# Kernel tuning notes

Measured on AMD Instinct MI355X. Metric: run time of the kernel, lower is better.

Reference implementation:

```python
import jax, jax.numpy as jnp
import numpy as np

D_MODEL = 256
NEG_INF = -1e9  # matches masked_fill value in the torch module


def setup_inputs() -> dict:
    key = jax.random.key(0)
    ks = jax.random.split(key, 7)
    B, S, D = 4, 4096, D_MODEL
    enc_q = jax.random.normal(ks[0], (B, S, D), dtype=jnp.float32)
    enc_k = jax.random.normal(ks[1], (B, S, D), dtype=jnp.float32)
    enc_v = jax.random.normal(ks[2], (B, S, D), dtype=jnp.float32)
    mask = jax.random.randint(ks[3], (B, S, S), 0, 2).astype(jnp.bool_)
    scale = 1.0 / np.sqrt(D)
    W_q = jax.random.normal(ks[4], (D, D), dtype=jnp.float32) * scale
    W_k = jax.random.normal(ks[5], (D, D), dtype=jnp.float32) * scale
    W_v = jax.random.normal(ks[6], (D, D), dtype=jnp.float32) * scale
    return {"encodings_q": enc_q, "encodings_k": enc_k, "encodings_v": enc_v,
            "mask": mask, "W_q": W_q, "W_k": W_k, "W_v": W_v}


def reference(encodings_q, encodings_k, encodings_v, mask, W_q, W_k, W_v):
    # nn.Linear(bias=False): y = x @ W^T
    q = jnp.einsum('bsd,ed->bse', encodings_q, W_q)
    k = jnp.einsum('bsd,ed->bse', encodings_k, W_k)
    v = jnp.einsum('bsd,ed->bse', encodings_v, W_v)
    sims = jnp.einsum('bqd,bkd->bqk', q, k) / jnp.sqrt(jnp.float32(D_MODEL))
    sims = jnp.where(mask, jnp.float32(NEG_INF), sims)
    attn = jax.nn.softmax(sims, axis=-1)
    return jnp.einsum('bqk,bkd->bqd', attn, v)
```

## Files before the change

kernel.cpp:

```cpp
#include <hip/hip_runtime.h>
#include <hip/hip_bf16.h>
#include <stdint.h>


typedef __attribute__((ext_vector_type(8))) short bf16x8;
typedef __attribute__((ext_vector_type(4))) float f32x4;

__device__ __forceinline__ short f2bf(float f) {
    union { float f; uint32_t u; } v; v.f = f;
    uint32_t r = v.u + 0x7FFFu + ((v.u >> 16) & 1u);
    return (short)(r >> 16);
}
__device__ __forceinline__ float bf2f(short s) {
    union { uint32_t u; float f; } v; v.u = ((uint32_t)(uint16_t)s) << 16;
    return v.f;
}

__global__ __launch_bounds__(512, 2)
void proj_kernel(const float* __restrict__ encq,
                 const float* __restrict__ enck,
                 const float* __restrict__ encv,
                 const float* __restrict__ Wq,
                 const float* __restrict__ Wk,
                 const float* __restrict__ Wv,
                 short* __restrict__ q_out,
                 short* __restrict__ k_out,
                 short* __restrict__ vt_out)
{
    __shared__ short As[128][72];
    __shared__ short Bs[256][72];

    const int tid = threadIdx.x;
    const int wave = tid >> 6, lane = tid & 63, lo = lane & 15, hi = lane >> 4;
    const int proj = blockIdx.y;
    const int row0 = blockIdx.x * 128;

    const float* X = (proj == 0) ? encq : (proj == 1) ? enck : encv;
    const float* W = (proj == 0) ? Wq   : (proj == 1) ? Wk   : Wv;

    f32x4 acc[16];
    #pragma unroll
    for (int n = 0; n < 16; ++n) {
        f32x4 z = {0.f, 0.f, 0.f, 0.f};
        acc[n] = z;
    }

    for (int ks = 0; ks < 4; ++ks) {
        const int k0 = ks * 64;
        __syncthreads();
        #pragma unroll
        for (int i = 0; i < 4; ++i) {
            int u = tid + i * 512;
            int r = u >> 4, c4 = u & 15;
            float4 v = *(const float4*)(X + (size_t)(row0 + r) * 256 + k0 + c4 * 4);
            short* dst = &As[r][c4 * 4];
            dst[0] = f2bf(v.x); dst[1] = f2bf(v.y); dst[2] = f2bf(v.z); dst[3] = f2bf(v.w);
        }
        #pragma unroll
        for (int i = 0; i < 8; ++i) {
            int u = tid + i * 512;
            int r = u >> 4, c4 = u & 15;
            float4 v = *(const float4*)(W + (size_t)r * 256 + k0 + c4 * 4);
            short* dst = &Bs[r][c4 * 4];
            dst[0] = f2bf(v.x); dst[1] = f2bf(v.y); dst[2] = f2bf(v.z); dst[3] = f2bf(v.w);
        }
        __syncthreads();
        #pragma unroll
        for (int kl = 0; kl < 2; ++kl) {
            bf16x8 a = *(const bf16x8*)&As[wave * 16 + lo][kl * 32 + hi * 8];
            #pragma unroll
            for (int n = 0; n < 16; ++n) {
                bf16x8 b = *(const bf16x8*)&Bs[n * 16 + lo][kl * 32 + hi * 8];
                acc[n] = __builtin_amdgcn_mfma_f32_16x16x32_bf16(a, b, acc[n], 0, 0, 0);
            }
        }
    }

    #pragma unroll
    for (int n = 0; n < 16; ++n)
        #pragma unroll
        for (int j = 0; j < 4; ++j) {
            int srow = row0 + wave * 16 + hi * 4 + j;
            int e = n * 16 + lo;
            float v = acc[n][j];
            if (proj == 0) {
                q_out[(size_t)srow * 256 + e] = f2bf(v * 0.0625f);
            } else if (proj == 1) {
                k_out[(size_t)srow * 256 + e] = f2bf(v);
            } else {
                int b = srow >> 12, s = srow & 4095;
                vt_out[((size_t)b * 256 + e) * 4096 + s] = f2bf(v);
            }
        }
}

__global__ __launch_bounds__(512, 2)
void attn_kernel(const short* __restrict__ qs,
                 const short* __restrict__ kk_,
                 const short* __restrict__ vt,
                 const int*   __restrict__ mask,
                 short* __restrict__ Opart,
                 float* __restrict__ Mpart,
                 float* __restrict__ Lpart)
{
    __shared__ short Ks[64 * 256];
    __shared__ short Vs[256 * 64];
    __shared__ short Ps[8][16][40];
    __shared__ unsigned long long Mb[128];

    const int tid = threadIdx.x;
    const int wave = tid >> 6, lane = tid & 63, lo = lane & 15, hi = lane >> 4;
    const int qt = blockIdx.x, b = blockIdx.y, split = blockIdx.z;
    const int qrow0 = qt * 128 + wave * 16;
    const size_t qg0 = (size_t)b * 4096 + qrow0;
    const int kv0 = split * 1024;

    bf16x8 qf[8];
    #pragma unroll
    for (int kk = 0; kk < 8; ++kk)
        qf[kk] = *(const bf16x8*)(qs + (qg0 + lo) * 256 + kk * 32 + hi * 8);

    f32x4 oacc[16];
    #pragma unroll
    for (int n = 0; n < 16; ++n) {
        f32x4 z = {0.f, 0.f, 0.f, 0.f};
        oacc[n] = z;
    }
    float Mst[4], Lst[4];
    #pragma unroll
    for (int j = 0; j < 4; ++j) { Mst[j] = -1e30f; Lst[j] = 0.f; }

    bf16x8 onesf;
    #pragma unroll
    for (int i = 0; i < 8; ++i) onesf[i] = (short)0x3F80;

    const short* ksrc0 = kk_ + ((size_t)b * 4096 + kv0) * 256;
    const size_t vbase = (size_t)b * 256 * 4096;
    const int mrow = tid >> 2, mpart = tid & 3;
    const int* msrc0 = mask + (size_t)b * 4096 * 4096
                     + (size_t)(qt * 128 + mrow) * 4096 + kv0 + mpart * 16;

    bf16x8 kreg[4], vreg[4];
    int4 mreg[4];
    #pragma unroll
    for (int i = 0; i < 4; ++i) {
        int u = tid + i * 512;
        kreg[i] = *(const bf16x8*)(ksrc0 + u * 8);
    }
    #pragma unroll
    for (int i = 0; i < 4; ++i) {
        int u = tid + i * 512;
        int r = u >> 3, cu = u & 7;
        vreg[i] = *(const bf16x8*)(vt + vbase + (size_t)r * 4096 + kv0 + cu * 8);
    }
    #pragma unroll
    for (int i = 0; i < 4; ++i)
        mreg[i] = *(const int4*)(msrc0 + i * 4);

    for (int t = 0; t < 16; ++t) {
        __syncthreads();
        #pragma unroll
        for (int i = 0; i < 4; ++i) {
            int u = tid + i * 512;
            int row = u >> 5, unit = u & 31;
            *(bf16x8*)&Ks[row * 256 + (unit ^ (row & 7)) * 8] = kreg[i];
        }
        #pragma unroll
        for (int i = 0; i < 4; ++i) {
            int u = tid + i * 512;
            int r = u >> 3, cu = u & 7;
            *(bf16x8*)&Vs[r * 64 + (cu ^ (r & 7)) * 8] = vreg[i];
        }
        {
            uint32_t mb = 0;
            #pragma unroll
            for (int i = 0; i < 4; ++i) {
                mb |= (uint32_t)(mreg[i].x != 0) << (i * 4);
                mb |= (uint32_t)(mreg[i].y != 0) << (i * 4 + 1);
                mb |= (uint32_t)(mreg[i].z != 0) << (i * 4 + 2);
                mb |= (uint32_t)(mreg[i].w != 0) << (i * 4 + 3);
            }
            ((unsigned short*)&Mb[mrow])[mpart] = (unsigned short)mb;
        }
        __syncthreads();

        if (t < 15) {
            const short* src = ksrc0 + (size_t)(t + 1) * 64 * 256;
            #pragma unroll
            for (int i = 0; i < 4; ++i) {
                int u = tid + i * 512;
                kreg[i] = *(const bf16x8*)(src + u * 8);
            }
            const int c0 = kv0 + (t + 1) * 64;
            #pragma unroll
            for (int i = 0; i < 4; ++i) {
                int u = tid + i * 512;
                int r = u >> 3, cu = u & 7;
                vreg[i] = *(const bf16x8*)(vt + vbase + (size_t)r * 4096 + c0 + cu * 8);
            }
            const int* ms = msrc0 + (t + 1) * 64;
            #pragma unroll
            for (int i = 0; i < 4; ++i)
                mreg[i] = *(const int4*)(ms + i * 4);
        }

        unsigned long long wls[4];
        #pragma unroll
        for (int j = 0; j < 4; ++j)
            wls[j] = Mb[wave * 16 + hi * 4 + j] >> lo;

        f32x4 sacc[4];
        #pragma unroll
        for (int n = 0; n < 4; ++n) {
            f32x4 z = {0.f, 0.f, 0.f, 0.f};
            sacc[n] = z;
        }
        #pragma unroll
        for (int kk = 0; kk < 8; ++kk) {
            #pragma unroll
            for (int n = 0; n < 4; ++n) {
                int row = n * 16 + lo;
                bf16x8 bk = *(const bf16x8*)&Ks[row * 256 + ((kk * 4 + hi) ^ (lo & 7)) * 8];
                sacc[n] = __builtin_amdgcn_mfma_f32_16x16x32_bf16(qf[kk], bk, sacc[n], 0, 0, 0);
            }
        }

        float ml[4];
        #pragma unroll
        for (int j = 0; j < 4; ++j) {
            float mx = -1e30f;
            #pragma unroll
            for (int n = 0; n < 4; ++n) {
                float s = sacc[n][j];
                if ((wls[j] >> (n * 16)) & 1ull) s = -1e30f;
                mx = fmaxf(mx, s);
            }
            #pragma unroll
            for (int d = 1; d < 16; d <<= 1)
                mx = fmaxf(mx, __shfl_xor(mx, d));
            ml[j] = mx;
        }

        bool needl = false;
        #pragma unroll
        for (int j = 0; j < 4; ++j)
            needl = needl || (ml[j] > Mst[j] + 8.0f);
        if (__any((int)needl)) {
            #pragma unroll
            for (int j = 0; j < 4; ++j) {
                float Mn = fmaxf(Mst[j], ml[j]);
                float sc = __expf(Mst[j] - Mn);
                Mst[j] = Mn;
                Lst[j] *= sc;
                #pragma unroll
                for (int n = 0; n < 16; ++n) oacc[n][j] *= sc;
            }
        }

        f32x4 lacc = {0.f, 0.f, 0.f, 0.f};
        #pragma unroll
        for (int g = 0; g < 2; ++g) {
            #pragma unroll
            for (int nn = 0; nn < 2; ++nn) {
                int n = g * 2 + nn;
                #pragma unroll
                for (int j = 0; j < 4; ++j) {
                    float p = __expf(sacc[n][j] - Mst[j]);
                    if ((wls[j] >> (n * 16)) & 1ull) p = 0.0f;
                    Ps[wave][hi * 4 + j][nn * 16 + lo] = f2bf(p);
                }
            }
            bf16x8 a2 = *(const bf16x8*)&Ps[wave][lo][hi * 8];
            #pragma unroll
            for (int n = 0; n < 16; ++n) {
                int row = n * 16 + lo;
                bf16x8 bv = *(const bf16x8*)&Vs[row * 64 + ((g * 4 + hi) ^ (lo & 7)) * 8];
                oacc[n] = __builtin_amdgcn_mfma_f32_16x16x32_bf16(a2, bv, oacc[n], 0, 0, 0);
            }
            lacc = __builtin_amdgcn_mfma_f32_16x16x32_bf16(a2, onesf, lacc, 0, 0, 0);
        }
        #pragma unroll
        for (int j = 0; j < 4; ++j)
            Lst[j] += lacc[j];
    }

    const size_t obase = ((size_t)split * 16384 + qg0) * 256;
    #pragma unroll
    for (int n = 0; n < 16; ++n)
        #pragma unroll
        for (int j = 0; j < 4; ++j)
            Opart[obase + (size_t)(hi * 4 + j) * 256 + n * 16 + lo] = f2bf(oacc[n][j]);
    if (lo == 0) {
        #pragma unroll
        for (int j = 0; j < 4; ++j) {
            size_t r = (size_t)split * 16384 + qg0 + hi * 4 + j;
            Mpart[r] = Mst[j];
            Lpart[r] = Lst[j];
        }
    }
}

__global__ __launch_bounds__(256)
void combine_kernel(const short* __restrict__ Opart,
                    const float* __restrict__ Mpart,
                    const float* __restrict__ Lpart,
                    float* __restrict__ out)
{
    int gid = blockIdx.x * 256 + threadIdx.x;
    int row = gid >> 6, c4 = gid & 63;
    float Ms[4], Ls[4], M = -1e30f;
    #pragma unroll
    for (int sp = 0; sp < 4; ++sp) {
        Ms[sp] = Mpart[sp * 16384 + row];
        Ls[sp] = Lpart[sp * 16384 + row];
        M = fmaxf(M, Ms[sp]);
    }
    float w[4], denom = 0.f;
    #pragma unroll
    for (int sp = 0; sp < 4; ++sp) {
        w[sp] = __expf(Ms[sp] - M);
        denom += w[sp] * Ls[sp];
    }
    float inv = 1.0f / denom;
    float4 r = {0.f, 0.f, 0.f, 0.f};
    #pragma unroll
    for (int sp = 0; sp < 4; ++sp) {
        short4 o = *(const short4*)(Opart + ((size_t)sp * 16384 + row) * 256 + c4 * 4);
        r.x += w[sp] * bf2f(o.x);
        r.y += w[sp] * bf2f(o.y);
        r.z += w[sp] * bf2f(o.z);
        r.w += w[sp] * bf2f(o.w);
    }
    r.x *= inv; r.y *= inv; r.z *= inv; r.w *= inv;
    *(float4*)(out + (size_t)row * 256 + c4 * 4) = r;
}

extern "C" void kernel_launch(void* const* d_in, const int* in_sizes, int n_in,
                              void* d_out, int out_size, void* d_ws, size_t ws_size,
                              hipStream_t stream)
{
    const float* encq = (const float*)d_in[0];
    const float* enck = (const float*)d_in[1];
    const float* encv = (const float*)d_in[2];
    const int*   mask = (const int*)d_in[3];
    const float* Wq   = (const float*)d_in[4];
    const float* Wk   = (const float*)d_in[5];
    const float* Wv   = (const float*)d_in[6];

    char* ws = (char*)d_ws;
    short* q_ws  = (short*)(ws);
    short* k_ws  = (short*)(ws + 8388608);
    short* vt_ws = (short*)(ws + 16777216);
    short* Opart = (short*)(ws + 25165824);
    float* Mpart = (float*)(ws + 58720256);
    float* Lpart = (float*)(ws + 58982400);
    float* out   = (float*)d_out;

    hipLaunchKernelGGL(proj_kernel, dim3(128, 3), dim3(512), 0, stream,
                       encq, enck, encv, Wq, Wk, Wv, q_ws, k_ws, vt_ws);
    hipLaunchKernelGGL(attn_kernel, dim3(32, 4, 4), dim3(512), 0, stream,
                       q_ws, k_ws, vt_ws, mask, Opart, Mpart, Lpart);
    hipLaunchKernelGGL(combine_kernel, dim3(4096), dim3(256), 0, stream,
                       Opart, Mpart, Lpart, out);
}
```

Baseline: 193.9 us.

## Double-buffer K/V/mask tiles in LDS with one barrier per iteration

```diff
diff --git a/kernel.cpp b/kernel.cpp
--- a/kernel.cpp
+++ b/kernel.cpp
@@ -103,10 +103,10 @@
                  float* __restrict__ Mpart,
                  float* __restrict__ Lpart)
 {
-    __shared__ short Ks[64 * 256];
-    __shared__ short Vs[256 * 64];
+    __shared__ short Ks[2][64 * 256];
+    __shared__ short Vs[2][256 * 64];
     __shared__ short Ps[8][16][40];
-    __shared__ unsigned long long Mb[128];
+    __shared__ unsigned long long Mb[2][128];
 
     const int tid = threadIdx.x;
     const int wave = tid >> 6, lane = tid & 63, lo = lane & 15, hi = lane >> 4;
@@ -142,72 +142,63 @@
 
     bf16x8 kreg[4], vreg[4];
     int4 mreg[4];
-    #pragma unroll
-    for (int i = 0; i < 4; ++i) {
-        int u = tid + i * 512;
-        kreg[i] = *(const bf16x8*)(ksrc0 + u * 8);
-    }
-    #pragma unroll
-    for (int i = 0; i < 4; ++i) {
-        int u = tid + i * 512;
-        int r = u >> 3, cu = u & 7;
-        vreg[i] = *(const bf16x8*)(vt + vbase + (size_t)r * 4096 + kv0 + cu * 8);
-    }
-    #pragma unroll
-    for (int i = 0; i < 4; ++i)
-        mreg[i] = *(const int4*)(msrc0 + i * 4);
+
+    auto load_regs = [&](int t) {
+        const short* src = ksrc0 + (size_t)t * 64 * 256;
+        #pragma unroll
+        for (int i = 0; i < 4; ++i) {
+            int u = tid + i * 512;
+            kreg[i] = *(const bf16x8*)(src + u * 8);
+        }
+        const int c0 = kv0 + t * 64;
+        #pragma unroll
+        for (int i = 0; i < 4; ++i) {
+            int u = tid + i * 512;
+            int r = u >> 3, cu = u & 7;
+            vreg[i] = *(const bf16x8*)(vt + vbase + (size_t)r * 4096 + c0 + cu * 8);
+        }
+        const int* ms = msrc0 + (size_t)t * 64;
+        #pragma unroll
+        for (int i = 0; i < 4; ++i)
+            mreg[i] = *(const int4*)(ms + i * 4);
+    };
+
+    auto commit = [&](int bi) {
+        #pragma unroll
+        for (int i = 0; i < 4; ++i) {
+            int u = tid + i * 512;
+            int row = u >> 5, unit = u & 31;
+            *(bf16x8*)&Ks[bi][row * 256 + (unit ^ (row & 7)) * 8] = kreg[i];
+        }
+        #pragma unroll
+        for (int i = 0; i < 4; ++i) {
+            int u = tid + i * 512;
+            int r = u >> 3, cu = u & 7;
+            *(bf16x8*)&Vs[bi][r * 64 + (cu ^ (r & 7)) * 8] = vreg[i];
+        }
+        uint32_t mb = 0;
+        #pragma unroll
+        for (int i = 0; i < 4; ++i) {
+            mb |= (uint32_t)(mreg[i].x != 0) << (i * 4);
+            mb |= (uint32_t)(mreg[i].y != 0) << (i * 4 + 1);
+            mb |= (uint32_t)(mreg[i].z != 0) << (i * 4 + 2);
+            mb |= (uint32_t)(mreg[i].w != 0) << (i * 4 + 3);
+        }
+        ((unsigned short*)&Mb[bi][mrow])[mpart] = (unsigned short)mb;
+    };
+
+    load_regs(0);
+    commit(0);
+    load_regs(1);
+    __syncthreads();
 
     for (int t = 0; t < 16; ++t) {
-        __syncthreads();
-        #pragma unroll
-        for (int i = 0; i < 4; ++i) {
-            int u = tid + i * 512;
-            int row = u >> 5, unit = u & 31;
-            *(bf16x8*)&Ks[row * 256 + (unit ^ (row & 7)) * 8] = kreg[i];
-        }
-        #pragma unroll
-        for (int i = 0; i < 4; ++i) {
-            int u = tid + i * 512;
-            int r = u >> 3, cu = u & 7;
-            *(bf16x8*)&Vs[r * 64 + (cu ^ (r & 7)) * 8] = vreg[i];
-        }
-        {
-            uint32_t mb = 0;
-            #pragma unroll
-            for (int i = 0; i < 4; ++i) {
-                mb |= (uint32_t)(mreg[i].x != 0) << (i * 4);
-                mb |= (uint32_t)(mreg[i].y != 0) << (i * 4 + 1);
-                mb |= (uint32_t)(mreg[i].z != 0) << (i * 4 + 2);
-                mb |= (uint32_t)(mreg[i].w != 0) << (i * 4 + 3);
-            }
-            ((unsigned short*)&Mb[mrow])[mpart] = (unsigned short)mb;
-        }
-        __syncthreads();
-
-        if (t < 15) {
-            const short* src = ksrc0 + (size_t)(t + 1) * 64 * 256;
-            #pragma unroll
-            for (int i = 0; i < 4; ++i) {
-                int u = tid + i * 512;
-                kreg[i] = *(const bf16x8*)(src + u * 8);
-            }
-            const int c0 = kv0 + (t + 1) * 64;
-            #pragma unroll
-            for (int i = 0; i < 4; ++i) {
-                int u = tid + i * 512;
-                int r = u >> 3, cu = u & 7;
-                vreg[i] = *(const bf16x8*)(vt + vbase + (size_t)r * 4096 + c0 + cu * 8);
-            }
-            const int* ms = msrc0 + (t + 1) * 64;
-            #pragma unroll
-            for (int i = 0; i < 4; ++i)
-                mreg[i] = *(const int4*)(ms + i * 4);
-        }
+        const int bi = t & 1;
 
         unsigned long long wls[4];
         #pragma unroll
         for (int j = 0; j < 4; ++j)
-            wls[j] = Mb[wave * 16 + hi * 4 + j] >> lo;
+            wls[j] = Mb[bi][wave * 16 + hi * 4 + j] >> lo;
 
         f32x4 sacc[4];
         #pragma unroll
@@ -220,7 +211,7 @@
             #pragma unroll
             for (int n = 0; n < 4; ++n) {
                 int row = n * 16 + lo;
-                bf16x8 bk = *(const bf16x8*)&Ks[row * 256 + ((kk * 4 + hi) ^ (lo & 7)) * 8];
+                bf16x8 bk = *(const bf16x8*)&Ks[bi][row * 256 + ((kk * 4 + hi) ^ (lo & 7)) * 8];
                 sacc[n] = __builtin_amdgcn_mfma_f32_16x16x32_bf16(qf[kk], bk, sacc[n], 0, 0, 0);
             }
         }
@@ -274,7 +265,7 @@
             #pragma unroll
             for (int n = 0; n < 16; ++n) {
                 int row = n * 16 + lo;
-                bf16x8 bv = *(const bf16x8*)&Vs[row * 64 + ((g * 4 + hi) ^ (lo & 7)) * 8];
+                bf16x8 bv = *(const bf16x8*)&Vs[bi][row * 64 + ((g * 4 + hi) ^ (lo & 7)) * 8];
                 oacc[n] = __builtin_amdgcn_mfma_f32_16x16x32_bf16(a2, bv, oacc[n], 0, 0, 0);
             }
             lacc = __builtin_amdgcn_mfma_f32_16x16x32_bf16(a2, onesf, lacc, 0, 0, 0);
@@ -282,6 +273,10 @@
         #pragma unroll
         for (int j = 0; j < 4; ++j)
             Lst[j] += lacc[j];
+
+        if (t < 15) commit(bi ^ 1);
+        if (t < 14) load_regs(t + 2);
+        __syncthreads();
     }
 
     const size_t obase = ((size_t)split * 16384 + qg0) * 256;
```

Result: slower. 211.3 us (+9.0%).
